# Optimization experiments

Measured on AMD Instinct MI355X. Metric: run time of the kernel, lower is better.

## Reference

```python
import jax, jax.numpy as jnp
import numpy as np

N = 50000      # nodes
E = 1_600_000  # edges per metapath graph
M = 3          # meta-path patterns
D = 128        # feature dim (in_size == out_size, GraphConv has no weight)
H = 128        # semantic-attention hidden size


def setup_inputs() -> dict:
    key = jax.random.key(0)
    k1, k2, k3, k4 = jax.random.split(key, 4)
    h = jax.random.normal(k1, (N, D), dtype=jnp.float32)
    # edges[m, 0] = src node ids, edges[m, 1] = dst node ids for metapath m
    edges = jax.random.randint(k2, (M, 2, E), 0, N, dtype=jnp.int32)
    W1 = jax.random.normal(k3, (D, H), dtype=jnp.float32) * 0.05
    b1 = jnp.zeros((H,), dtype=jnp.float32)
    W2 = jax.random.normal(k4, (H, 1), dtype=jnp.float32) * 0.05
    return {"h": h, "edges": edges, "W1": W1, "b1": b1, "W2": W2}


def _graph_conv_both(h, src, dst, n):
    """DGL GraphConv(norm='both', weight=None, bias=None):
    out = D_in^{-1/2} * A @ (D_out^{-1/2} * h), zero degrees clamped to 1."""
    ones = jnp.ones_like(src, dtype=h.dtype)
    out_deg = jax.ops.segment_sum(ones, src, num_segments=n)
    in_deg = jax.ops.segment_sum(ones, dst, num_segments=n)
    norm_src = jax.lax.rsqrt(jnp.maximum(out_deg, 1.0))
    norm_dst = jax.lax.rsqrt(jnp.maximum(in_deg, 1.0))
    msg = (h * norm_src[:, None])[src]                  # [E, D] gather
    agg = jax.ops.segment_sum(msg, dst, num_segments=n)  # [N, D] scatter-add
    return agg * norm_dst[:, None]


def reference(h, edges, W1, b1, W2):
    n = h.shape[0]
    m = edges.shape[0]
    # One normalized sparse aggregation per meta-path (fixed small M).
    z = jnp.stack(
        [_graph_conv_both(h, edges[i, 0], edges[i, 1], n) for i in range(m)],
        axis=1,
    )  # [N, M, D]
    # Semantic attention: project -> tanh -> score, mean over nodes, softmax over M.
    w = jnp.mean(jnp.tanh(z @ W1 + b1) @ W2, axis=0)  # [M, 1]
    beta = jax.nn.softmax(w, axis=0)                  # [M, 1]
    return jnp.sum(beta[None, :, :] * z, axis=1)      # [N, D]
```

## Files before the change

### kernel.cpp

```cpp
#include <hip/hip_runtime.h>
#include <cstdint>
#include <cstddef>

typedef unsigned int  uint;
typedef unsigned short ushort;
typedef short bf16x8 __attribute__((ext_vector_type(8)));
typedef float f32x4  __attribute__((ext_vector_type(4)));

#define N_NODES 50000
#define N_EDGES 1600000
#define N_META  3
#define DIM     128

#define BKT       256
#define NBKT      196
#define BIN_CHUNK 16384
#define NCHUNK    98
#define CSR_CAP   10240
#define OCH       128
#define EPC       (N_EDGES / OCH)
#define OWORDS    12500
#define PREP_A    (N_META * OCH)
#define W1C_B     4

#define AT_TILE   64
#define AT_NBLK   782

__device__ __forceinline__ uint bf16rne(float f) {
    const uint u = __float_as_uint(f);
    return (u + 0x7FFFu + ((u >> 16) & 1u)) >> 16;
}
__device__ __forceinline__ float bflo(uint p) { return __uint_as_float(p << 16); }
__device__ __forceinline__ float bfhi(uint p) { return __uint_as_float(p & 0xFFFF0000u); }
__device__ __forceinline__ float fast_tanh(float x) {
    const float e = __expf(2.0f * x);
    return 1.0f - 2.0f / (e + 1.0f);
}

__global__ __launch_bounds__(256) void prep_kernel(
        const int* __restrict__ edges, const float* __restrict__ W1,
        int* __restrict__ bucket_cnt, uint* __restrict__ partials,
        ushort* __restrict__ W1T) {
    __shared__ __align__(16) uint sh[OWORDS];
    __shared__ uint bh[NBKT];
    const int blk = blockIdx.x;
    if (blk < PREP_A) {
        const int m = blk >> 7, c = blk & 127;
        uint4* sh4 = reinterpret_cast<uint4*>(sh);
        for (int j = threadIdx.x; j < OWORDS / 4; j += 256)
            sh4[j] = make_uint4(0u, 0u, 0u, 0u);
        for (int j = threadIdx.x; j < NBKT; j += 256) bh[j] = 0;
        __syncthreads();
        const int* src = edges + (size_t)(2 * m) * N_EDGES;
        const int* dst = edges + (size_t)(2 * m + 1) * N_EDGES;
        const int beg = c * EPC, end = beg + EPC;
        for (int i = beg + 4 * threadIdx.x; i + 4 <= end; i += 1024) {
            const uint4 s4 = *reinterpret_cast<const uint4*>(src + i);
            const uint4 d4 = *reinterpret_cast<const uint4*>(dst + i);
            atomicAdd(&sh[s4.x >> 2], 1u << (8 * (s4.x & 3)));
            atomicAdd(&sh[s4.y >> 2], 1u << (8 * (s4.y & 3)));
            atomicAdd(&sh[s4.z >> 2], 1u << (8 * (s4.z & 3)));
            atomicAdd(&sh[s4.w >> 2], 1u << (8 * (s4.w & 3)));
            atomicAdd(&bh[d4.x >> 8], 1u);
            atomicAdd(&bh[d4.y >> 8], 1u);
            atomicAdd(&bh[d4.z >> 8], 1u);
            atomicAdd(&bh[d4.w >> 8], 1u);
        }
        __syncthreads();
        uint4* outp4 = reinterpret_cast<uint4*>(
            partials + (size_t)(m * OCH + c) * OWORDS);
        for (int j = threadIdx.x; j < OWORDS / 4; j += 256) outp4[j] = sh4[j];
        for (int j = threadIdx.x; j < NBKT; j += 256)
            if (bh[j]) atomicAdd(&bucket_cnt[m * NBKT + j], (int)bh[j]);
    } else {
        const int base = (blk - PREP_A) * (DIM * DIM / W1C_B);
        for (int o = base + threadIdx.x; o < base + DIM * DIM / W1C_B; o += 256) {
            const int j = o >> 7, k = o & 127;
            W1T[o] = (ushort)bf16rne(W1[k * DIM + j]);
        }
    }
}

__global__ __launch_bounds__(256) void scan_nsrc_kernel(
        const int* __restrict__ bucket_cnt, int* __restrict__ bucket_off,
        int* __restrict__ bucket_cur, int* __restrict__ row_off,
        const uint* __restrict__ partials, float* __restrict__ nsrc) {
    const int blk = blockIdx.x;
    if (blk < N_META) {
        __shared__ int sc[256];
        const int m = blk, t = threadIdx.x;
        const int v = (t < NBKT) ? bucket_cnt[m * NBKT + t] : 0;
        sc[t] = v;
        __syncthreads();
        for (int off = 1; off < 256; off <<= 1) {
            const int tt = (t >= off) ? sc[t - off] : 0;
            __syncthreads();
            sc[t] += tt;
            __syncthreads();
        }
        const int excl = sc[t] - v;
        if (t < NBKT) {
            bucket_off[m * (NBKT + 1) + t] = excl;
            bucket_cur[m * NBKT + t] = excl;
        }
        if (t == 0) {
            bucket_off[m * (NBKT + 1) + NBKT] = N_EDGES;
            row_off[m * (N_NODES + 1) + N_NODES] = N_EDGES;
        }
    } else {
        const int i = (blk - N_META) * 256 + threadIdx.x;
        if (i < N_META * N_NODES) {
            const int m = i / N_NODES, node = i - m * N_NODES;
            const int q = node >> 2, s8 = 8 * (node & 3);
            int s = 0;
#pragma unroll 8
            for (int c = 0; c < OCH; ++c)
                s += (partials[(size_t)(m * OCH + c) * OWORDS + q] >> s8) & 0xFF;
            nsrc[i] = rsqrtf(fmaxf((float)s, 1.0f));
        }
    }
}

__global__ __launch_bounds__(256) void scale_kernel(
        const float* __restrict__ h, const float* __restrict__ nsrc,
        ushort* __restrict__ hbm) {
    const int i = blockIdx.x * 256 + threadIdx.x;
    const int node = i >> 5;
    const float4 v = reinterpret_cast<const float4*>(h)[i];
    uint2* o = reinterpret_cast<uint2*>(hbm);
#pragma unroll
    for (int m = 0; m < N_META; ++m) {
        const float n = nsrc[m * N_NODES + node];
        uint2 p;
        p.x = bf16rne(v.x * n) | (bf16rne(v.y * n) << 16);
        p.y = bf16rne(v.z * n) | (bf16rne(v.w * n) << 16);
        o[(size_t)m * (N_NODES * DIM / 4) + i] = p;
    }
}

__global__ __launch_bounds__(256) void bin_kernel(
        const int* __restrict__ edges, int* __restrict__ bucket_cur,
        uint* __restrict__ pairs) {
    const int m = blockIdx.y;
    __shared__ int hist[NBKT];
    __shared__ int cur[NBKT];
    for (int j = threadIdx.x; j < NBKT; j += 256) hist[j] = 0;
    __syncthreads();
    const int* src = edges + (size_t)(2 * m) * N_EDGES;
    const int* dst = edges + (size_t)(2 * m + 1) * N_EDGES;
    const int beg = blockIdx.x * BIN_CHUNK;
    const int end = min(beg + BIN_CHUNK, N_EDGES);
    for (int i = beg + 4 * threadIdx.x; i + 4 <= end; i += 1024) {
        const uint4 d4 = *reinterpret_cast<const uint4*>(dst + i);
        atomicAdd(&hist[d4.x >> 8], 1);
        atomicAdd(&hist[d4.y >> 8], 1);
        atomicAdd(&hist[d4.z >> 8], 1);
        atomicAdd(&hist[d4.w >> 8], 1);
    }
    __syncthreads();
    for (int j = threadIdx.x; j < NBKT; j += 256) {
        const int n = hist[j];
        cur[j] = n ? atomicAdd(&bucket_cur[m * NBKT + j], n) : 0;
    }
    __syncthreads();
    uint* pm = pairs + (size_t)m * N_EDGES;
    for (int i = beg + 4 * threadIdx.x; i + 4 <= end; i += 1024) {
        const uint4 s4 = *reinterpret_cast<const uint4*>(src + i);
        const uint4 d4 = *reinterpret_cast<const uint4*>(dst + i);
        int p0 = atomicAdd(&cur[d4.x >> 8], 1);
        pm[p0] = (d4.x << 16) | s4.x;
        int p1 = atomicAdd(&cur[d4.y >> 8], 1);
        pm[p1] = (d4.y << 16) | s4.y;
        int p2 = atomicAdd(&cur[d4.z >> 8], 1);
        pm[p2] = (d4.z << 16) | s4.z;
        int p3 = atomicAdd(&cur[d4.w >> 8], 1);
        pm[p3] = (d4.w << 16) | s4.w;
    }
}

__global__ __launch_bounds__(256) void csr_kernel(
        const uint* __restrict__ pairs, const int* __restrict__ bucket_off,
        int* __restrict__ row_off, ushort* __restrict__ csr) {
    const int b = blockIdx.x, m = blockIdx.y;
    const int node_base = b * BKT;
    const int nb = min(BKT, N_NODES - node_base);
    __shared__ uint stage[CSR_CAP];
    __shared__ int hist[BKT];
    __shared__ int sc[BKT];
    __shared__ int cur[BKT];
    hist[threadIdx.x] = 0;
    __syncthreads();
    const int beg = bucket_off[m * (NBKT + 1) + b];
    const int end = bucket_off[m * (NBKT + 1) + b + 1];
    const int cnt = end - beg;
    const uint* pm = pairs + (size_t)m * N_EDGES + beg;
    for (int i = threadIdx.x; i < cnt; i += 256) {
        const uint p = pm[i];
        if (i < CSR_CAP) stage[i] = p;
        atomicAdd(&hist[(int)(p >> 16) - node_base], 1);
    }
    __syncthreads();
    const int v = hist[threadIdx.x];
    sc[threadIdx.x] = v;
    __syncthreads();
    for (int off = 1; off < BKT; off <<= 1) {
        const int t = (threadIdx.x >= off) ? sc[threadIdx.x - off] : 0;
        __syncthreads();
        sc[threadIdx.x] += t;
        __syncthreads();
    }
    const int excl = sc[threadIdx.x] - v;
    cur[threadIdx.x] = beg + excl;
    if (threadIdx.x < nb)
        row_off[m * (N_NODES + 1) + node_base + threadIdx.x] = beg + excl;
    __syncthreads();
    ushort* cm = csr + (size_t)m * N_EDGES;
    for (int i = threadIdx.x; i < cnt; i += 256) {
        const uint p = (i < CSR_CAP) ? stage[i] : pm[i];
        const int dl = (int)(p >> 16) - node_base;
        const int pos = atomicAdd(&cur[dl], 1);
        cm[pos] = (ushort)(p & 0xFFFFu);
    }
}

__global__ __launch_bounds__(256) void gather_kernel(
        const ushort* __restrict__ hbm, const ushort* __restrict__ csr,
        const int* __restrict__ row_off, ushort* __restrict__ zb) {
    const int m    = blockIdx.y;
    const int wave = threadIdx.x >> 6;
    const int lane = threadIdx.x & 63;
    const int q    = lane >> 4;
    const int c16  = lane & 15;
    const int node = blockIdx.x * 4 + wave;
    const int* ro = row_off + m * (N_NODES + 1);
    const int beg = ro[node];
    const int end = ro[node + 1];
    const ushort* srcs = csr + (size_t)m * N_EDGES;
    const ushort* tab  = hbm + (size_t)m * N_NODES * DIM;
    float acc[8] = {};
    int j = beg;
    for (; j + 16 <= end; j += 16) {
        int s[4]; uint4 hv[4];
#pragma unroll
        for (int u = 0; u < 4; ++u) s[u] = srcs[j + 4 * u + q];
#pragma unroll
        for (int u = 0; u < 4; ++u)
            hv[u] = *reinterpret_cast<const uint4*>(tab + (size_t)s[u] * DIM + c16 * 8);
#pragma unroll
        for (int u = 0; u < 4; ++u) {
            acc[0] += bflo(hv[u].x); acc[1] += bfhi(hv[u].x);
            acc[2] += bflo(hv[u].y); acc[3] += bfhi(hv[u].y);
            acc[4] += bflo(hv[u].z); acc[5] += bfhi(hv[u].z);
            acc[6] += bflo(hv[u].w); acc[7] += bfhi(hv[u].w);
        }
    }
    for (; j + 4 <= end; j += 4) {
        const int s0 = srcs[j + q];
        const uint4 hv = *reinterpret_cast<const uint4*>(tab + (size_t)s0 * DIM + c16 * 8);
        acc[0] += bflo(hv.x); acc[1] += bfhi(hv.x);
        acc[2] += bflo(hv.y); acc[3] += bfhi(hv.y);
        acc[4] += bflo(hv.z); acc[5] += bfhi(hv.z);
        acc[6] += bflo(hv.w); acc[7] += bfhi(hv.w);
    }
    if (j + q < end) {
        const int s0 = srcs[j + q];
        const uint4 hv = *reinterpret_cast<const uint4*>(tab + (size_t)s0 * DIM + c16 * 8);
        acc[0] += bflo(hv.x); acc[1] += bfhi(hv.x);
        acc[2] += bflo(hv.y); acc[3] += bfhi(hv.y);
        acc[4] += bflo(hv.z); acc[5] += bfhi(hv.z);
        acc[6] += bflo(hv.w); acc[7] += bfhi(hv.w);
    }
#pragma unroll
    for (int k = 0; k < 8; ++k) {
        acc[k] += __shfl_xor(acc[k], 16);
        acc[k] += __shfl_xor(acc[k], 32);
    }
    if (lane < 16) {
        const float nd = rsqrtf(fmaxf((float)(end - beg), 1.0f));
        uint4 o;
        o.x = bf16rne(acc[0] * nd) | (bf16rne(acc[1] * nd) << 16);
        o.y = bf16rne(acc[2] * nd) | (bf16rne(acc[3] * nd) << 16);
        o.z = bf16rne(acc[4] * nd) | (bf16rne(acc[5] * nd) << 16);
        o.w = bf16rne(acc[6] * nd) | (bf16rne(acc[7] * nd) << 16);
        *reinterpret_cast<uint4*>(
            zb + ((size_t)m * N_NODES + node) * DIM + c16 * 8) = o;
    }
}

__global__ __launch_bounds__(256) void attn_kernel(
        const ushort* __restrict__ zb, const ushort* __restrict__ W1T,
        const float* __restrict__ b1, const float* __restrict__ W2,
        float* __restrict__ wacc) {
    const int m   = blockIdx.y;
    const int tid = threadIdx.x;
    const int wv  = tid >> 6;
    const int l   = tid & 63;
    __shared__ __align__(16) ushort w1s[DIM * DIM];
    __shared__ float red[4];

    {
        const uint4* g = reinterpret_cast<const uint4*>(W1T);
        for (int i = tid; i < DIM * DIM / 8; i += 256) {
            const int j = i >> 4;
            const int slot = i ^ (j & 7);
            *reinterpret_cast<uint4*>(
                reinterpret_cast<char*>(w1s) + slot * 16) =
                g[i];
        }
    }
    __syncthreads();

    const int node_base = blockIdx.x * AT_TILE + wv * 16;
    const int row = l & 15;
    const int q   = l >> 4;
    int nload = node_base + row;
    if (nload >= N_NODES) nload = N_NODES - 1;
    const ushort* zrow = zb + ((size_t)m * N_NODES + nload) * DIM + q * 8;

    bf16x8 a[4];
#pragma unroll
    for (int kk = 0; kk < 4; ++kk)
        a[kk] = *reinterpret_cast<const bf16x8*>(zrow + kk * 32);

    f32x4 acc[8];
#pragma unroll
    for (int ct = 0; ct < 8; ++ct) acc[ct] = (f32x4){0.f, 0.f, 0.f, 0.f};

#pragma unroll
    for (int kk = 0; kk < 4; ++kk) {
#pragma unroll
        for (int ct = 0; ct < 8; ++ct) {
            const int j = ct * 16 + row;
            const int slot = (j * 16 + kk * 4 + q) ^ (j & 7);
            const bf16x8 b = *reinterpret_cast<const bf16x8*>(
                reinterpret_cast<char*>(w1s) + slot * 16);
            acc[ct] = __builtin_amdgcn_mfma_f32_16x16x32_bf16(
                a[kk], b, acc[ct], 0, 0, 0);
        }
    }

    float local = 0.0f;
#pragma unroll
    for (int ct = 0; ct < 8; ++ct) {
        const int j = ct * 16 + row;
        const float b1j = b1[j];
        const float w2j = W2[j];
#pragma unroll
        for (int r = 0; r < 4; ++r) {
            const int nd = node_base + q * 4 + r;
            if (nd < N_NODES)
                local += fast_tanh(acc[ct][r] + b1j) * w2j;
        }
    }
    for (int off = 32; off > 0; off >>= 1)
        local += __shfl_xor(local, off);
    if (l == 0) red[wv] = local;
    __syncthreads();
    if (tid == 0)
        atomicAdd(&wacc[m], red[0] + red[1] + red[2] + red[3]);
}

__global__ __launch_bounds__(256) void final_kernel(
        const ushort* __restrict__ zb, const float* __restrict__ wacc,
        float* __restrict__ out) {
    const int g = blockIdx.x * 256 + threadIdx.x;
    const float invN = 1.0f / (float)N_NODES;
    const float w0 = wacc[0] * invN, w1 = wacc[1] * invN, w2 = wacc[2] * invN;
    const float mx = fmaxf(w0, fmaxf(w1, w2));
    const float e0 = expf(w0 - mx), e1 = expf(w1 - mx), e2 = expf(w2 - mx);
    const float inv = 1.0f / (e0 + e1 + e2);
    const float beta[3] = {e0 * inv, e1 * inv, e2 * inv};
    float a[8] = {};
#pragma unroll
    for (int m = 0; m < N_META; ++m) {
        const uint4 v = reinterpret_cast<const uint4*>(zb)[
            (size_t)m * (N_NODES * DIM / 8) + g];
        const float bm = beta[m];
        a[0] = fmaf(bflo(v.x), bm, a[0]); a[1] = fmaf(bfhi(v.x), bm, a[1]);
        a[2] = fmaf(bflo(v.y), bm, a[2]); a[3] = fmaf(bfhi(v.y), bm, a[3]);
        a[4] = fmaf(bflo(v.z), bm, a[4]); a[5] = fmaf(bfhi(v.z), bm, a[5]);
        a[6] = fmaf(bflo(v.w), bm, a[6]); a[7] = fmaf(bfhi(v.w), bm, a[7]);
    }
    float4 o0 = {a[0], a[1], a[2], a[3]};
    float4 o1 = {a[4], a[5], a[6], a[7]};
    reinterpret_cast<float4*>(out)[(size_t)g * 2 + 0] = o0;
    reinterpret_cast<float4*>(out)[(size_t)g * 2 + 1] = o1;
}

extern "C" void kernel_launch(void* const* d_in, const int* in_sizes, int n_in,
                              void* d_out, int out_size, void* d_ws, size_t ws_size,
                              hipStream_t stream) {
    const float* h    = (const float*)d_in[0];
    const int*  edges = (const int*)d_in[1];
    const float* W1   = (const float*)d_in[2];
    const float* b1   = (const float*)d_in[3];
    const float* W2   = (const float*)d_in[4];
    float* out = (float*)d_out;

    char* p = (char*)d_ws;
    ushort* zb      = (ushort*)p;
    uint*  pairs    = (uint*)p;
    uint*  partials = (uint*)(p + (size_t)N_META * N_EDGES * 4);
    p += (size_t)N_META * N_NODES * DIM * 2;
    ushort* hbm     = (ushort*)p; p += (size_t)N_META * N_NODES * DIM * 2;
    ushort* csr     = (ushort*)p; p += (size_t)N_META * N_EDGES * 2;
    int* row_off    = (int*)p;    p += ((size_t)N_META * (N_NODES + 1) + 1) * 4;
    float* nsrc     = (float*)p;  p += (size_t)N_META * N_NODES * 4;
    float* wacc     = (float*)p;  p += 16 * 4;
    int* bucket_cnt = (int*)p;    p += (size_t)N_META * NBKT * 4;
    int* bucket_off = (int*)p;    p += (size_t)N_META * (NBKT + 1) * 4 + 4;
    int* bucket_cur = (int*)p;    p += (size_t)N_META * NBKT * 4;
    ushort* W1T     = (ushort*)p; p += (size_t)DIM * DIM * 2;

    hipMemsetAsync(wacc, 0, (16 + (size_t)N_META * NBKT) * 4, stream);

    prep_kernel<<<dim3(PREP_A + W1C_B), 256, 0, stream>>>(
        edges, W1, bucket_cnt, partials, W1T);
    scan_nsrc_kernel<<<dim3(N_META + (N_META * N_NODES + 255) / 256), 256, 0, stream>>>(
        bucket_cnt, bucket_off, bucket_cur, row_off, partials, nsrc);
    scale_kernel<<<dim3(N_NODES * DIM / 4 / 256), 256, 0, stream>>>(h, nsrc, hbm);
    bin_kernel<<<dim3(NCHUNK, N_META), 256, 0, stream>>>(edges, bucket_cur, pairs);
    csr_kernel<<<dim3(NBKT, N_META), 256, 0, stream>>>(pairs, bucket_off, row_off, csr);
    gather_kernel<<<dim3(N_NODES / 4, N_META), 256, 0, stream>>>(
        hbm, csr, row_off, zb);
    attn_kernel<<<dim3(AT_NBLK, N_META), 256, 0, stream>>>(zb, W1T, b1, W2, wacc);
    final_kernel<<<dim3(N_NODES * DIM / 8 / 256), 256, 0, stream>>>(zb, wacc, out);
}
```

Before: 383.0 us.

## Build CSR via per-node in-degree scan and direct atomic scatter

Result: slower. 849.9 us (+121.9%).

```diff
diff --git a/kernel.cpp b/kernel.cpp
--- a/kernel.cpp
+++ b/kernel.cpp
@@ -12,11 +12,8 @@
 #define N_META  3
 #define DIM     128
 
-#define BKT       256
-#define NBKT      196
 #define BIN_CHUNK 16384
 #define NCHUNK    98
-#define CSR_CAP   10240
 #define OCH       128
 #define EPC       (N_EDGES / OCH)
 #define OWORDS    12500
@@ -26,6 +23,9 @@
 #define AT_TILE   64
 #define AT_NBLK   782
 
+#define SCB       1024
+#define NPT       49
+
 __device__ __forceinline__ uint bf16rne(float f) {
     const uint u = __float_as_uint(f);
     return (u + 0x7FFFu + ((u >> 16) & 1u)) >> 16;
@@ -39,41 +39,34 @@
 
 __global__ __launch_bounds__(256) void prep_kernel(
         const int* __restrict__ edges, const float* __restrict__ W1,
-        int* __restrict__ bucket_cnt, uint* __restrict__ partials,
+        uint* __restrict__ partials_out, uint* __restrict__ partials_in,
         ushort* __restrict__ W1T) {
     __shared__ __align__(16) uint sh[OWORDS];
-    __shared__ uint bh[NBKT];
     const int blk = blockIdx.x;
-    if (blk < PREP_A) {
-        const int m = blk >> 7, c = blk & 127;
+    if (blk < 2 * PREP_A) {
+        const int isdst = (blk >= PREP_A) ? 1 : 0;
+        const int b = blk - isdst * PREP_A;
+        const int m = b >> 7, c = b & 127;
         uint4* sh4 = reinterpret_cast<uint4*>(sh);
         for (int j = threadIdx.x; j < OWORDS / 4; j += 256)
             sh4[j] = make_uint4(0u, 0u, 0u, 0u);
-        for (int j = threadIdx.x; j < NBKT; j += 256) bh[j] = 0;
         __syncthreads();
-        const int* src = edges + (size_t)(2 * m) * N_EDGES;
-        const int* dst = edges + (size_t)(2 * m + 1) * N_EDGES;
-        const int beg = c * EPC, end = beg + EPC;
-        for (int i = beg + 4 * threadIdx.x; i + 4 <= end; i += 1024) {
-            const uint4 s4 = *reinterpret_cast<const uint4*>(src + i);
-            const uint4 d4 = *reinterpret_cast<const uint4*>(dst + i);
-            atomicAdd(&sh[s4.x >> 2], 1u << (8 * (s4.x & 3)));
-            atomicAdd(&sh[s4.y >> 2], 1u << (8 * (s4.y & 3)));
-            atomicAdd(&sh[s4.z >> 2], 1u << (8 * (s4.z & 3)));
-            atomicAdd(&sh[s4.w >> 2], 1u << (8 * (s4.w & 3)));
-            atomicAdd(&bh[d4.x >> 8], 1u);
-            atomicAdd(&bh[d4.y >> 8], 1u);
-            atomicAdd(&bh[d4.z >> 8], 1u);
-            atomicAdd(&bh[d4.w >> 8], 1u);
+        const int* ids = edges + ((size_t)(2 * m) + isdst) * N_EDGES;
+        const int beg = c * EPC;
+        for (int i = beg + 4 * threadIdx.x; i + 4 <= beg + EPC; i += 1024) {
+            const uint4 v = *reinterpret_cast<const uint4*>(ids + i);
+            atomicAdd(&sh[v.x >> 2], 1u << (8 * (v.x & 3)));
+            atomicAdd(&sh[v.y >> 2], 1u << (8 * (v.y & 3)));
+            atomicAdd(&sh[v.z >> 2], 1u << (8 * (v.z & 3)));
+            atomicAdd(&sh[v.w >> 2], 1u << (8 * (v.w & 3)));
         }
         __syncthreads();
-        uint4* outp4 = reinterpret_cast<uint4*>(
-            partials + (size_t)(m * OCH + c) * OWORDS);
-        for (int j = threadIdx.x; j < OWORDS / 4; j += 256) outp4[j] = sh4[j];
-        for (int j = threadIdx.x; j < NBKT; j += 256)
-            if (bh[j]) atomicAdd(&bucket_cnt[m * NBKT + j], (int)bh[j]);
+        uint* base = (isdst ? partials_in : partials_out)
+                   + (size_t)(m * OCH + c) * OWORDS;
+        uint4* out4 = reinterpret_cast<uint4*>(base);
+        for (int j = threadIdx.x; j < OWORDS / 4; j += 256) out4[j] = sh4[j];
     } else {
-        const int base = (blk - PREP_A) * (DIM * DIM / W1C_B);
+        const int base = (blk - 2 * PREP_A) * (DIM * DIM / W1C_B);
         for (int o = base + threadIdx.x; o < base + DIM * DIM / W1C_B; o += 256) {
             const int j = o >> 7, k = o & 127;
             W1T[o] = (ushort)bf16rne(W1[k * DIM + j]);
@@ -81,44 +74,56 @@
     }
 }
 
-__global__ __launch_bounds__(256) void scan_nsrc_kernel(
-        const int* __restrict__ bucket_cnt, int* __restrict__ bucket_off,
-        int* __restrict__ bucket_cur, int* __restrict__ row_off,
-        const uint* __restrict__ partials, float* __restrict__ nsrc) {
-    const int blk = blockIdx.x;
-    if (blk < N_META) {
-        __shared__ int sc[256];
-        const int m = blk, t = threadIdx.x;
-        const int v = (t < NBKT) ? bucket_cnt[m * NBKT + t] : 0;
-        sc[t] = v;
+__global__ __launch_bounds__(256) void deg_kernel(
+        const uint* __restrict__ partials_out,
+        const uint* __restrict__ partials_in,
+        float* __restrict__ nsrc, int* __restrict__ in_deg) {
+    const int i = blockIdx.x * 256 + threadIdx.x;
+    if (i >= N_META * N_NODES) return;
+    const int m = i / N_NODES, node = i - m * N_NODES;
+    const int q = node >> 2, s8 = 8 * (node & 3);
+    int so = 0, si = 0;
+#pragma unroll 8
+    for (int c = 0; c < OCH; ++c) {
+        so += (partials_out[(size_t)(m * OCH + c) * OWORDS + q] >> s8) & 0xFF;
+        si += (partials_in [(size_t)(m * OCH + c) * OWORDS + q] >> s8) & 0xFF;
+    }
+    nsrc[i] = rsqrtf(fmaxf((float)so, 1.0f));
+    in_deg[i] = si;
+}
+
+__global__ __launch_bounds__(1024) void rowoff_kernel(
+        const int* __restrict__ in_deg, int* __restrict__ row_off,
+        int* __restrict__ cur) {
+    __shared__ int sc[SCB];
+    const int m = blockIdx.x, t = threadIdx.x;
+    const int base = t * NPT;
+    const int* dm = in_deg + m * N_NODES;
+    int s = 0;
+    for (int i = 0; i < NPT; ++i) {
+        const int n = base + i;
+        if (n < N_NODES) s += dm[n];
+    }
+    sc[t] = s;
+    __syncthreads();
+    for (int off = 1; off < SCB; off <<= 1) {
+        const int tt = (t >= off) ? sc[t - off] : 0;
         __syncthreads();
-        for (int off = 1; off < 256; off <<= 1) {
-            const int tt = (t >= off) ? sc[t - off] : 0;
-            __syncthreads();
-            sc[t] += tt;
-            __syncthreads();
-        }
-        const int excl = sc[t] - v;
-        if (t < NBKT) {
-            bucket_off[m * (NBKT + 1) + t] = excl;
-            bucket_cur[m * NBKT + t] = excl;
-        }
-        if (t == 0) {
-            bucket_off[m * (NBKT + 1) + NBKT] = N_EDGES;
-            row_off[m * (N_NODES + 1) + N_NODES] = N_EDGES;
-        }
-    } else {
-        const int i = (blk - N_META) * 256 + threadIdx.x;
-        if (i < N_META * N_NODES) {
-            const int m = i / N_NODES, node = i - m * N_NODES;
-            const int q = node >> 2, s8 = 8 * (node & 3);
-            int s = 0;
-#pragma unroll 8
-            for (int c = 0; c < OCH; ++c)
-                s += (partials[(size_t)(m * OCH + c) * OWORDS + q] >> s8) & 0xFF;
-            nsrc[i] = rsqrtf(fmaxf((float)s, 1.0f));
-        }
-    }
+        sc[t] += tt;
+        __syncthreads();
+    }
+    int run = sc[t] - s;
+    int* ro = row_off + m * (N_NODES + 1);
+    int* cm = cur + m * N_NODES;
+    for (int i = 0; i < NPT; ++i) {
+        const int n = base + i;
+        if (n < N_NODES) {
+            ro[n] = run;
+            cm[n] = run;
+            run += dm[n];
+        }
+    }
+    if (t == 0) ro[N_NODES] = N_EDGES;
 }
 
 __global__ __launch_bounds__(256) void scale_kernel(
@@ -138,88 +143,23 @@
     }
 }
 
-__global__ __launch_bounds__(256) void bin_kernel(
-        const int* __restrict__ edges, int* __restrict__ bucket_cur,
-        uint* __restrict__ pairs) {
+__global__ __launch_bounds__(256) void scatter_kernel(
+        const int* __restrict__ edges, int* __restrict__ cur,
+        ushort* __restrict__ csr) {
     const int m = blockIdx.y;
-    __shared__ int hist[NBKT];
-    __shared__ int cur[NBKT];
-    for (int j = threadIdx.x; j < NBKT; j += 256) hist[j] = 0;
-    __syncthreads();
     const int* src = edges + (size_t)(2 * m) * N_EDGES;
     const int* dst = edges + (size_t)(2 * m + 1) * N_EDGES;
     const int beg = blockIdx.x * BIN_CHUNK;
     const int end = min(beg + BIN_CHUNK, N_EDGES);
-    for (int i = beg + 4 * threadIdx.x; i + 4 <= end; i += 1024) {
-        const uint4 d4 = *reinterpret_cast<const uint4*>(dst + i);
-        atomicAdd(&hist[d4.x >> 8], 1);
-        atomicAdd(&hist[d4.y >> 8], 1);
-        atomicAdd(&hist[d4.z >> 8], 1);
-        atomicAdd(&hist[d4.w >> 8], 1);
-    }
-    __syncthreads();
-    for (int j = threadIdx.x; j < NBKT; j += 256) {
-        const int n = hist[j];
-        cur[j] = n ? atomicAdd(&bucket_cur[m * NBKT + j], n) : 0;
-    }
-    __syncthreads();
-    uint* pm = pairs + (size_t)m * N_EDGES;
+    int* cm = cur + m * N_NODES;
+    ushort* out = csr + (size_t)m * N_EDGES;
     for (int i = beg + 4 * threadIdx.x; i + 4 <= end; i += 1024) {
         const uint4 s4 = *reinterpret_cast<const uint4*>(src + i);
         const uint4 d4 = *reinterpret_cast<const uint4*>(dst + i);
-        int p0 = atomicAdd(&cur[d4.x >> 8], 1);
-        pm[p0] = (d4.x << 16) | s4.x;
-        int p1 = atomicAdd(&cur[d4.y >> 8], 1);
-        pm[p1] = (d4.y << 16) | s4.y;
-        int p2 = atomicAdd(&cur[d4.z >> 8], 1);
-        pm[p2] = (d4.z << 16) | s4.z;
-        int p3 = atomicAdd(&cur[d4.w >> 8], 1);
-        pm[p3] = (d4.w << 16) | s4.w;
-    }
-}
-
-__global__ __launch_bounds__(256) void csr_kernel(
-        const uint* __restrict__ pairs, const int* __restrict__ bucket_off,
-        int* __restrict__ row_off, ushort* __restrict__ csr) {
-    const int b = blockIdx.x, m = blockIdx.y;
-    const int node_base = b * BKT;
-    const int nb = min(BKT, N_NODES - node_base);
-    __shared__ uint stage[CSR_CAP];
-    __shared__ int hist[BKT];
-    __shared__ int sc[BKT];
-    __shared__ int cur[BKT];
-    hist[threadIdx.x] = 0;
-    __syncthreads();
-    const int beg = bucket_off[m * (NBKT + 1) + b];
-    const int end = bucket_off[m * (NBKT + 1) + b + 1];
-    const int cnt = end - beg;
-    const uint* pm = pairs + (size_t)m * N_EDGES + beg;
-    for (int i = threadIdx.x; i < cnt; i += 256) {
-        const uint p = pm[i];
-        if (i < CSR_CAP) stage[i] = p;
-        atomicAdd(&hist[(int)(p >> 16) - node_base], 1);
-    }
-    __syncthreads();
-    const int v = hist[threadIdx.x];
-    sc[threadIdx.x] = v;
-    __syncthreads();
-    for (int off = 1; off < BKT; off <<= 1) {
-        const int t = (threadIdx.x >= off) ? sc[threadIdx.x - off] : 0;
-        __syncthreads();
-        sc[threadIdx.x] += t;
-        __syncthreads();
-    }
-    const int excl = sc[threadIdx.x] - v;
-    cur[threadIdx.x] = beg + excl;
-    if (threadIdx.x < nb)
-        row_off[m * (N_NODES + 1) + node_base + threadIdx.x] = beg + excl;
-    __syncthreads();
-    ushort* cm = csr + (size_t)m * N_EDGES;
-    for (int i = threadIdx.x; i < cnt; i += 256) {
-        const uint p = (i < CSR_CAP) ? stage[i] : pm[i];
-        const int dl = (int)(p >> 16) - node_base;
-        const int pos = atomicAdd(&cur[dl], 1);
-        cm[pos] = (ushort)(p & 0xFFFFu);
+        out[atomicAdd(&cm[d4.x], 1)] = (ushort)s4.x;
+        out[atomicAdd(&cm[d4.y], 1)] = (ushort)s4.y;
+        out[atomicAdd(&cm[d4.z], 1)] = (ushort)s4.z;
+        out[atomicAdd(&cm[d4.w], 1)] = (ushort)s4.w;
     }
 }
 
@@ -304,8 +244,7 @@
             const int j = i >> 4;
             const int slot = i ^ (j & 7);
             *reinterpret_cast<uint4*>(
-                reinterpret_cast<char*>(w1s) + slot * 16) =
-                g[i];
+                reinterpret_cast<char*>(w1s) + slot * 16) = g[i];
         }
     }
     __syncthreads();
@@ -398,29 +337,28 @@
     float* out = (float*)d_out;
 
     char* p = (char*)d_ws;
-    ushort* zb      = (ushort*)p;
-    uint*  pairs    = (uint*)p;
-    uint*  partials = (uint*)(p + (size_t)N_META * N_EDGES * 4);
+    ushort* zb           = (ushort*)p;
+    uint*  partials_out  = (uint*)p;
+    uint*  partials_in   = (uint*)(p + (size_t)N_META * OCH * OWORDS * 4);
     p += (size_t)N_META * N_NODES * DIM * 2;
     ushort* hbm     = (ushort*)p; p += (size_t)N_META * N_NODES * DIM * 2;
     ushort* csr     = (ushort*)p; p += (size_t)N_META * N_EDGES * 2;
     int* row_off    = (int*)p;    p += ((size_t)N_META * (N_NODES + 1) + 1) * 4;
     float* nsrc     = (float*)p;  p += (size_t)N_META * N_NODES * 4;
+    int* in_deg     = (int*)p;    p += (size_t)N_META * N_NODES * 4;
+    int* cur        = (int*)p;    p += (size_t)N_META * N_NODES * 4;
     float* wacc     = (float*)p;  p += 16 * 4;
-    int* bucket_cnt = (int*)p;    p += (size_t)N_META * NBKT * 4;
-    int* bucket_off = (int*)p;    p += (size_t)N_META * (NBKT + 1) * 4 + 4;
-    int* bucket_cur = (int*)p;    p += (size_t)N_META * NBKT * 4;
     ushort* W1T     = (ushort*)p; p += (size_t)DIM * DIM * 2;
 
-    hipMemsetAsync(wacc, 0, (16 + (size_t)N_META * NBKT) * 4, stream);
-
-    prep_kernel<<<dim3(PREP_A + W1C_B), 256, 0, stream>>>(
-        edges, W1, bucket_cnt, partials, W1T);
-    scan_nsrc_kernel<<<dim3(N_META + (N_META * N_NODES + 255) / 256), 256, 0, stream>>>(
-        bucket_cnt, bucket_off, bucket_cur, row_off, partials, nsrc);
+    hipMemsetAsync(wacc, 0, 16 * 4, stream);
+
+    prep_kernel<<<dim3(2 * PREP_A + W1C_B), 256, 0, stream>>>(
+        edges, W1, partials_out, partials_in, W1T);
+    deg_kernel<<<dim3((N_META * N_NODES + 255) / 256), 256, 0, stream>>>(
+        partials_out, partials_in, nsrc, in_deg);
+    rowoff_kernel<<<dim3(N_META), SCB, 0, stream>>>(in_deg, row_off, cur);
     scale_kernel<<<dim3(N_NODES * DIM / 4 / 256), 256, 0, stream>>>(h, nsrc, hbm);
-    bin_kernel<<<dim3(NCHUNK, N_META), 256, 0, stream>>>(edges, bucket_cur, pairs);
-    csr_kernel<<<dim3(NBKT, N_META), 256, 0, stream>>>(pairs, bucket_off, row_off, csr);
+    scatter_kernel<<<dim3(NCHUNK, N_META), 256, 0, stream>>>(edges, cur, csr);
     gather_kernel<<<dim3(N_NODES / 4, N_META), 256, 0, stream>>>(
         hbm, csr, row_off, zb);
     attn_kernel<<<dim3(AT_NBLK, N_META), 256, 0, stream>>>(zb, W1T, b1, W2, wacc);
```

## Reuse per-chunk bucket histograms from prep to precompute bin offsets

Applied to the files above, without the earlier changes.

Measured after the change: 381.9 us. Within noise of the previous version (-0.3%).

```diff
diff --git a/kernel.cpp b/kernel.cpp
--- a/kernel.cpp
+++ b/kernel.cpp
@@ -14,8 +14,6 @@
 
 #define BKT       256
 #define NBKT      196
-#define BIN_CHUNK 16384
-#define NCHUNK    98
 #define CSR_CAP   10240
 #define OCH       128
 #define EPC       (N_EDGES / OCH)
@@ -39,7 +37,7 @@
 
 __global__ __launch_bounds__(256) void prep_kernel(
         const int* __restrict__ edges, const float* __restrict__ W1,
-        int* __restrict__ bucket_cnt, uint* __restrict__ partials,
+        uint* __restrict__ bhout, uint* __restrict__ partials,
         ushort* __restrict__ W1T) {
     __shared__ __align__(16) uint sh[OWORDS];
     __shared__ uint bh[NBKT];
@@ -53,8 +51,8 @@
         __syncthreads();
         const int* src = edges + (size_t)(2 * m) * N_EDGES;
         const int* dst = edges + (size_t)(2 * m + 1) * N_EDGES;
-        const int beg = c * EPC, end = beg + EPC;
-        for (int i = beg + 4 * threadIdx.x; i + 4 <= end; i += 1024) {
+        const int beg = c * EPC;
+        for (int i = beg + 4 * threadIdx.x; i + 4 <= beg + EPC; i += 1024) {
             const uint4 s4 = *reinterpret_cast<const uint4*>(src + i);
             const uint4 d4 = *reinterpret_cast<const uint4*>(dst + i);
             atomicAdd(&sh[s4.x >> 2], 1u << (8 * (s4.x & 3)));
@@ -70,8 +68,8 @@
         uint4* outp4 = reinterpret_cast<uint4*>(
             partials + (size_t)(m * OCH + c) * OWORDS);
         for (int j = threadIdx.x; j < OWORDS / 4; j += 256) outp4[j] = sh4[j];
-        for (int j = threadIdx.x; j < NBKT; j += 256)
-            if (bh[j]) atomicAdd(&bucket_cnt[m * NBKT + j], (int)bh[j]);
+        uint* bo = bhout + (size_t)(m * OCH + c) * NBKT;
+        for (int j = threadIdx.x; j < NBKT; j += 256) bo[j] = bh[j];
     } else {
         const int base = (blk - PREP_A) * (DIM * DIM / W1C_B);
         for (int o = base + threadIdx.x; o < base + DIM * DIM / W1C_B; o += 256) {
@@ -82,14 +80,17 @@
 }
 
 __global__ __launch_bounds__(256) void scan_nsrc_kernel(
-        const int* __restrict__ bucket_cnt, int* __restrict__ bucket_off,
-        int* __restrict__ bucket_cur, int* __restrict__ row_off,
+        const uint* __restrict__ bhout, int* __restrict__ bucket_off,
+        int* __restrict__ chunk_base, int* __restrict__ row_off,
         const uint* __restrict__ partials, float* __restrict__ nsrc) {
     const int blk = blockIdx.x;
     if (blk < N_META) {
         __shared__ int sc[256];
         const int m = blk, t = threadIdx.x;
-        const int v = (t < NBKT) ? bucket_cnt[m * NBKT + t] : 0;
+        int v = 0;
+        if (t < NBKT)
+            for (int c = 0; c < OCH; ++c)
+                v += (int)bhout[(size_t)(m * OCH + c) * NBKT + t];
         sc[t] = v;
         __syncthreads();
         for (int off = 1; off < 256; off <<= 1) {
@@ -101,7 +102,11 @@
         const int excl = sc[t] - v;
         if (t < NBKT) {
             bucket_off[m * (NBKT + 1) + t] = excl;
-            bucket_cur[m * NBKT + t] = excl;
+            int run = excl;
+            for (int c = 0; c < OCH; ++c) {
+                chunk_base[(size_t)(m * OCH + c) * NBKT + t] = run;
+                run += (int)bhout[(size_t)(m * OCH + c) * NBKT + t];
+            }
         }
         if (t == 0) {
             bucket_off[m * (NBKT + 1) + NBKT] = N_EDGES;
@@ -139,32 +144,18 @@
 }
 
 __global__ __launch_bounds__(256) void bin_kernel(
-        const int* __restrict__ edges, int* __restrict__ bucket_cur,
+        const int* __restrict__ edges, const int* __restrict__ chunk_base,
         uint* __restrict__ pairs) {
-    const int m = blockIdx.y;
-    __shared__ int hist[NBKT];
+    const int m = blockIdx.y, c = blockIdx.x;
     __shared__ int cur[NBKT];
-    for (int j = threadIdx.x; j < NBKT; j += 256) hist[j] = 0;
+    const int* cb = chunk_base + (size_t)(m * OCH + c) * NBKT;
+    for (int j = threadIdx.x; j < NBKT; j += 256) cur[j] = cb[j];
     __syncthreads();
     const int* src = edges + (size_t)(2 * m) * N_EDGES;
     const int* dst = edges + (size_t)(2 * m + 1) * N_EDGES;
-    const int beg = blockIdx.x * BIN_CHUNK;
-    const int end = min(beg + BIN_CHUNK, N_EDGES);
-    for (int i = beg + 4 * threadIdx.x; i + 4 <= end; i += 1024) {
-        const uint4 d4 = *reinterpret_cast<const uint4*>(dst + i);
-        atomicAdd(&hist[d4.x >> 8], 1);
-        atomicAdd(&hist[d4.y >> 8], 1);
-        atomicAdd(&hist[d4.z >> 8], 1);
-        atomicAdd(&hist[d4.w >> 8], 1);
-    }
-    __syncthreads();
-    for (int j = threadIdx.x; j < NBKT; j += 256) {
-        const int n = hist[j];
-        cur[j] = n ? atomicAdd(&bucket_cur[m * NBKT + j], n) : 0;
-    }
-    __syncthreads();
+    const int beg = c * EPC;
     uint* pm = pairs + (size_t)m * N_EDGES;
-    for (int i = beg + 4 * threadIdx.x; i + 4 <= end; i += 1024) {
+    for (int i = beg + 4 * threadIdx.x; i + 4 <= beg + EPC; i += 1024) {
         const uint4 s4 = *reinterpret_cast<const uint4*>(src + i);
         const uint4 d4 = *reinterpret_cast<const uint4*>(dst + i);
         int p0 = atomicAdd(&cur[d4.x >> 8], 1);
@@ -304,8 +295,7 @@
             const int j = i >> 4;
             const int slot = i ^ (j & 7);
             *reinterpret_cast<uint4*>(
-                reinterpret_cast<char*>(w1s) + slot * 16) =
-                g[i];
+                reinterpret_cast<char*>(w1s) + slot * 16) = g[i];
         }
     }
     __syncthreads();
@@ -407,19 +397,19 @@
     int* row_off    = (int*)p;    p += ((size_t)N_META * (N_NODES + 1) + 1) * 4;
     float* nsrc     = (float*)p;  p += (size_t)N_META * N_NODES * 4;
     float* wacc     = (float*)p;  p += 16 * 4;
-    int* bucket_cnt = (int*)p;    p += (size_t)N_META * NBKT * 4;
+    uint* bhout     = (uint*)p;   p += (size_t)N_META * OCH * NBKT * 4;
+    int* chunk_base = (int*)p;    p += (size_t)N_META * OCH * NBKT * 4;
     int* bucket_off = (int*)p;    p += (size_t)N_META * (NBKT + 1) * 4 + 4;
-    int* bucket_cur = (int*)p;    p += (size_t)N_META * NBKT * 4;
     ushort* W1T     = (ushort*)p; p += (size_t)DIM * DIM * 2;
 
-    hipMemsetAsync(wacc, 0, (16 + (size_t)N_META * NBKT) * 4, stream);
+    hipMemsetAsync(wacc, 0, 16 * 4, stream);
 
     prep_kernel<<<dim3(PREP_A + W1C_B), 256, 0, stream>>>(
-        edges, W1, bucket_cnt, partials, W1T);
+        edges, W1, bhout, partials, W1T);
     scan_nsrc_kernel<<<dim3(N_META + (N_META * N_NODES + 255) / 256), 256, 0, stream>>>(
-        bucket_cnt, bucket_off, bucket_cur, row_off, partials, nsrc);
+        bhout, bucket_off, chunk_base, row_off, partials, nsrc);
     scale_kernel<<<dim3(N_NODES * DIM / 4 / 256), 256, 0, stream>>>(h, nsrc, hbm);
-    bin_kernel<<<dim3(NCHUNK, N_META), 256, 0, stream>>>(edges, bucket_cur, pairs);
+    bin_kernel<<<dim3(OCH, N_META), 256, 0, stream>>>(edges, chunk_base, pairs);
     csr_kernel<<<dim3(NBKT, N_META), 256, 0, stream>>>(pairs, bucket_off, row_off, csr);
     gather_kernel<<<dim3(N_NODES / 4, N_META), 256, 0, stream>>>(
         hbm, csr, row_off, zb);
```
